# Kernel tuning notes

Measured on AMD Instinct MI355X. Metric: run time of the kernel, lower is better.

## Reference

```python
import jax, jax.numpy as jnp
import numpy as np

B = 4096
D = 2048
K = 8          # num_intention
H2 = 64        # fc2 out


def setup_inputs() -> dict:
    key = jax.random.key(0)
    ks = jax.random.split(key, 8)
    x = jax.random.normal(ks[0], (B, D), dtype=jnp.float32)
    # one-hot intention per sample
    idx = jax.random.randint(ks[1], (B,), 0, K)
    intention = jax.nn.one_hot(idx, K, dtype=jnp.float32)
    s1 = 1.0 / np.sqrt(D)
    s2 = 1.0 / np.sqrt(K)
    s3 = 1.0 / np.sqrt(D + H2)
    W1 = jax.random.uniform(ks[2], (D * K, D), jnp.float32, -s1, s1)
    b1 = jax.random.uniform(ks[3], (D * K,), jnp.float32, -s1, s1)
    W2 = jax.random.uniform(ks[4], (H2, K), jnp.float32, -s2, s2)
    b2 = jax.random.uniform(ks[5], (H2,), jnp.float32, -s2, s2)
    W3 = jax.random.uniform(ks[6], (1, D + H2), jnp.float32, -s3, s3)
    b3 = jax.random.uniform(ks[7], (1,), jnp.float32, -s3, s3)
    return {"x": x, "intention": intention, "W1": W1, "b1": b1,
            "W2": W2, "b2": b2, "W3": W3, "b3": b3}


def reference(x, intention, W1, b1, W2, b2, W3, b3):
    # fc2 on the one-hot intention -> [B, 64]
    y2 = intention @ W2.T + b2
    # fc1 densely computes all K branches (dropout treated as identity / eval mode)
    y1 = x @ W1.T + b1                      # [B, D*K]
    # mask = intention.repeat(1, 2048): branch axis is INNERMOST (interleaved)
    y1 = y1.reshape(B, D, K)                # [B, D, K]
    sel = jax.lax.stop_gradient(intention)  # mask is non-differentiable in torch
    y1 = jnp.einsum('bdk,bk->bd', y1, sel)  # gather active branch -> [B, D]
    y3 = jax.nn.relu(jnp.concatenate([y1, y2], axis=1))  # [B, D+64]
    y = y3 @ W3.T + b3                      # [B, 1]
    return y
```

## Files before the change

### kernel.cpp

```cpp
#include <hip/hip_runtime.h>
#include <hip/hip_bf16.h>
#include <stdint.h>

#define NB 4096
#define ND 2048
#define NK 8
#define NH 64

#define BM 128
#define BN 128
#define BK 32
#define MAX_ROWS 5120
#define MAX_TILES 40

typedef __bf16 bf16;
typedef __bf16 bf16x8 __attribute__((ext_vector_type(8)));
typedef float floatx4 __attribute__((ext_vector_type(4)));

#define OFF_KIDX   0u
#define OFF_ORDER  16384u
#define OFF_META   40960u
#define OFF_XG     65536u
#define OFF_WB     21037056u

__global__ void prep_kernel(const float* __restrict__ intention,
                            const float* __restrict__ W2,
                            const float* __restrict__ b2,
                            const float* __restrict__ W3,
                            const float* __restrict__ b3,
                            int* __restrict__ kidx,
                            int* __restrict__ order,
                            int* __restrict__ meta,
                            float* __restrict__ out)
{
    __shared__ int cnt[NK];
    __shared__ int cur[NK];
    __shared__ float c2s[NK];
    const int tid = threadIdx.x;

    if (tid < NK) cnt[tid] = 0;
    for (int i = tid; i < MAX_ROWS; i += 256) order[i] = -1;
    __syncthreads();

    for (int b = tid; b < NB; b += 256) {
        const float* row = intention + b * NK;
        int k = 0;
#pragma unroll
        for (int j = 1; j < NK; j++)
            if (row[j] > 0.5f) k = j;
        kidx[b] = k;
        atomicAdd(&cnt[k], 1);
    }
    __syncthreads();

    if (tid == 0) {
        int running = 0, nt = 0;
        for (int k = 0; k < NK; k++) {
            cur[k] = running;
            int ntile = (cnt[k] + BM - 1) / BM;
            for (int t = 0; t < ntile; t++) {
                meta[1 + nt] = k;
                meta[1 + MAX_TILES + nt] = running + t * BM;
                nt++;
            }
            running += ntile * BM;
        }
        meta[0] = nt;
    }
    __syncthreads();

    for (int b = tid; b < NB; b += 256) {
        int k = kidx[b];
        int pos = atomicAdd(&cur[k], 1);
        order[pos] = b;
    }

    if (tid < NK) {
        float s = b3[0];
        for (int h = 0; h < NH; h++) {
            float v = W2[h * NK + tid] + b2[h];
            if (v > 0.f) s += v * W3[ND + h];
        }
        c2s[tid] = s;
    }
    __syncthreads();

    for (int b = tid; b < NB; b += 256)
        out[b] = c2s[kidx[b]];
}

__global__ void gather_x_kernel(const float* __restrict__ x,
                                const int* __restrict__ order,
                                bf16* __restrict__ xg)
{
    const int row = blockIdx.x;
    const int t = threadIdx.x;
    const int b = order[row];
    bf16* dst = xg + (size_t)row * ND + t * 8;
    bf16x8 v;
    if (b < 0) {
#pragma unroll
        for (int i = 0; i < 8; i++) v[i] = (bf16)0.f;
    } else {
        const float* src = x + (size_t)b * ND + t * 8;
        float4 a = *(const float4*)(src);
        float4 c = *(const float4*)(src + 4);
        v[0] = (bf16)a.x; v[1] = (bf16)a.y; v[2] = (bf16)a.z; v[3] = (bf16)a.w;
        v[4] = (bf16)c.x; v[5] = (bf16)c.y; v[6] = (bf16)c.z; v[7] = (bf16)c.w;
    }
    *(bf16x8*)dst = v;
}

__global__ void conv_w1_kernel(const float* __restrict__ W1,
                               bf16* __restrict__ Wb)
{
    const int r = blockIdx.x;
    const int t = threadIdx.x;
    const int d = r >> 3;
    const int k = r & 7;
    const float* src = W1 + (size_t)r * ND + t * 8;
    bf16* dst = Wb + ((size_t)k * ND + d) * ND + t * 8;
    float4 a = *(const float4*)(src);
    float4 c = *(const float4*)(src + 4);
    bf16x8 v;
    v[0] = (bf16)a.x; v[1] = (bf16)a.y; v[2] = (bf16)a.z; v[3] = (bf16)a.w;
    v[4] = (bf16)c.x; v[5] = (bf16)c.y; v[6] = (bf16)c.z; v[7] = (bf16)c.w;
    *(bf16x8*)dst = v;
}

__global__ void gemm_kernel(const bf16* __restrict__ xg,
                            const bf16* __restrict__ Wb,
                            const int* __restrict__ order,
                            const int* __restrict__ meta,
                            const float* __restrict__ b1,
                            const float* __restrict__ W3,
                            float* __restrict__ out)
{
    const int n_mt = meta[0];
    const int mt = blockIdx.y;
    if (mt >= n_mt) return;
    const int kbr = meta[1 + mt];
    const int row0 = meta[1 + MAX_TILES + mt];
    const int col0 = blockIdx.x * BN;

    __shared__ bf16 As[BM * BK];
    __shared__ bf16 Bs[BN * BK];

    const int tid = threadIdx.x;
    const int lane = tid & 63;
    const int wid = tid >> 6;
    const int wm = wid >> 1;
    const int wn = wid & 1;

    const bf16* Abase = xg + (size_t)row0 * ND;
    const bf16* Bbase = Wb + ((size_t)kbr * ND + col0) * ND;

    const int srow = tid >> 2;
    const int scol = (tid & 3) * 8;

    floatx4 zero = {0.f, 0.f, 0.f, 0.f};
    floatx4 acc[4][4];
#pragma unroll
    for (int i = 0; i < 4; i++)
#pragma unroll
        for (int j = 0; j < 4; j++) acc[i][j] = zero;

    const int qk = (lane >> 4) * 8;
    const int mrow = lane & 15;

    for (int kk = 0; kk < ND; kk += BK) {
#pragma unroll
        for (int r = 0; r < 2; r++) {
            const bf16* ga = Abase + (size_t)(r * 64 + srow) * ND + kk + scol;
            const bf16* gb = Bbase + (size_t)(r * 64 + srow) * ND + kk + scol;
            bf16* la = As + r * 2048 + wid * 512;
            bf16* lb = Bs + r * 2048 + wid * 512;
            __builtin_amdgcn_global_load_lds(
                (const __attribute__((address_space(1))) void*)ga,
                (__attribute__((address_space(3))) void*)la, 16, 0, 0);
            __builtin_amdgcn_global_load_lds(
                (const __attribute__((address_space(1))) void*)gb,
                (__attribute__((address_space(3))) void*)lb, 16, 0, 0);
        }
        __syncthreads();

        bf16x8 af[4], bfv[4];
#pragma unroll
        for (int i = 0; i < 4; i++) {
            af[i]  = *(const bf16x8*)(As + (wm * 64 + i * 16 + mrow) * BK + qk);
            bfv[i] = *(const bf16x8*)(Bs + (wn * 64 + i * 16 + mrow) * BK + qk);
        }
#pragma unroll
        for (int i = 0; i < 4; i++)
#pragma unroll
            for (int j = 0; j < 4; j++)
                acc[i][j] = __builtin_amdgcn_mfma_f32_16x16x32_bf16(
                    af[i], bfv[j], acc[i][j], 0, 0, 0);
        __syncthreads();
    }

    const int colq = lane & 15;
    const int quad = lane >> 4;
    float bias[4], w3v[4];
#pragma unroll
    for (int j = 0; j < 4; j++) {
        int d = col0 + wn * 64 + j * 16 + colq;
        bias[j] = b1[d * NK + kbr];
        w3v[j] = W3[d];
    }
#pragma unroll
    for (int i = 0; i < 4; i++) {
#pragma unroll
        for (int r = 0; r < 4; r++) {
            float s = 0.f;
#pragma unroll
            for (int j = 0; j < 4; j++) {
                float v = acc[i][j][r] + bias[j];
                s += (v > 0.f) ? v * w3v[j] : 0.f;
            }
#pragma unroll
            for (int m = 1; m < 16; m <<= 1) s += __shfl_xor(s, m, 64);
            if (colq == 0) {
                int grow = row0 + wm * 64 + i * 16 + quad * 4 + r;
                int b = order[grow];
                if (b >= 0) atomicAdd(out + b, s);
            }
        }
    }
}

extern "C" void kernel_launch(void* const* d_in, const int* in_sizes, int n_in,
                              void* d_out, int out_size, void* d_ws, size_t ws_size,
                              hipStream_t stream)
{
    const float* x         = (const float*)d_in[0];
    const float* intention = (const float*)d_in[1];
    const float* W1        = (const float*)d_in[2];
    const float* b1        = (const float*)d_in[3];
    const float* W2        = (const float*)d_in[4];
    const float* b2        = (const float*)d_in[5];
    const float* W3        = (const float*)d_in[6];
    const float* b3        = (const float*)d_in[7];
    float* out = (float*)d_out;

    char* ws = (char*)d_ws;
    int*  kidx  = (int*)(ws + OFF_KIDX);
    int*  order = (int*)(ws + OFF_ORDER);
    int*  meta  = (int*)(ws + OFF_META);
    bf16* xg    = (bf16*)(ws + OFF_XG);
    bf16* Wb    = (bf16*)(ws + OFF_WB);

    prep_kernel<<<dim3(1), dim3(256), 0, stream>>>(
        intention, W2, b2, W3, b3, kidx, order, meta, out);
    conv_w1_kernel<<<dim3(NK * ND), dim3(256), 0, stream>>>(W1, Wb);
    gather_x_kernel<<<dim3(MAX_ROWS), dim3(256), 0, stream>>>(x, order, xg);
    gemm_kernel<<<dim3(ND / BN, MAX_TILES), dim3(256), 0, stream>>>(
        xg, Wb, order, meta, b1, W3, out);
}
```

Before: 338.0 us.

## Fuse fp32-to-bf16 conversion and row gather into GEMM tile loads

Removes the separate W1 conversion and x gather kernels; the GEMM now loads fp32 rows of x (via the sorted order) and the interleaved W1 rows directly, converts to bf16 in registers and stores into padded shared memory. This eliminates writing and rereading bf16 copies of W1 and x in global memory. It gives up the async global-to-LDS loads and reads twice the bytes per tile from fp32 sources, with W1 rows strided by the branch interleave. Shared memory rows are padded to reduce bank conflicts.

```diff
diff --git a/kernel.cpp b/kernel.cpp
--- a/kernel.cpp
+++ b/kernel.cpp
@@ -10,6 +10,7 @@
 #define BM 128
 #define BN 128
 #define BK 32
+#define LDA 40
 #define MAX_ROWS 5120
 #define MAX_TILES 40
 
@@ -20,8 +21,6 @@
 #define OFF_KIDX   0u
 #define OFF_ORDER  16384u
 #define OFF_META   40960u
-#define OFF_XG     65536u
-#define OFF_WB     21037056u
 
 __global__ void prep_kernel(const float* __restrict__ intention,
                             const float* __restrict__ W2,
@@ -89,47 +88,15 @@
         out[b] = c2s[kidx[b]];
 }
 
-__global__ void gather_x_kernel(const float* __restrict__ x,
-                                const int* __restrict__ order,
-                                bf16* __restrict__ xg)
-{
-    const int row = blockIdx.x;
-    const int t = threadIdx.x;
-    const int b = order[row];
-    bf16* dst = xg + (size_t)row * ND + t * 8;
-    bf16x8 v;
-    if (b < 0) {
-#pragma unroll
-        for (int i = 0; i < 8; i++) v[i] = (bf16)0.f;
-    } else {
-        const float* src = x + (size_t)b * ND + t * 8;
-        float4 a = *(const float4*)(src);
-        float4 c = *(const float4*)(src + 4);
-        v[0] = (bf16)a.x; v[1] = (bf16)a.y; v[2] = (bf16)a.z; v[3] = (bf16)a.w;
-        v[4] = (bf16)c.x; v[5] = (bf16)c.y; v[6] = (bf16)c.z; v[7] = (bf16)c.w;
-    }
-    *(bf16x8*)dst = v;
-}
-
-__global__ void conv_w1_kernel(const float* __restrict__ W1,
-                               bf16* __restrict__ Wb)
-{
-    const int r = blockIdx.x;
-    const int t = threadIdx.x;
-    const int d = r >> 3;
-    const int k = r & 7;
-    const float* src = W1 + (size_t)r * ND + t * 8;
-    bf16* dst = Wb + ((size_t)k * ND + d) * ND + t * 8;
-    float4 a = *(const float4*)(src);
-    float4 c = *(const float4*)(src + 4);
+__device__ inline void cvt_store16(bf16* dst, float4 a, float4 c) {
     bf16x8 v;
     v[0] = (bf16)a.x; v[1] = (bf16)a.y; v[2] = (bf16)a.z; v[3] = (bf16)a.w;
     v[4] = (bf16)c.x; v[5] = (bf16)c.y; v[6] = (bf16)c.z; v[7] = (bf16)c.w;
     *(bf16x8*)dst = v;
 }
 
-__global__ void gemm_kernel(const bf16* __restrict__ xg,
-                            const bf16* __restrict__ Wb,
+__global__ void gemm_kernel(const float* __restrict__ x,
+                            const float* __restrict__ W1,
                             const int* __restrict__ order,
                             const int* __restrict__ meta,
                             const float* __restrict__ b1,
@@ -143,8 +110,9 @@
     const int row0 = meta[1 + MAX_TILES + mt];
     const int col0 = blockIdx.x * BN;
 
-    __shared__ bf16 As[BM * BK];
-    __shared__ bf16 Bs[BN * BK];
+    __shared__ int rowb[BM];
+    __shared__ bf16 As[BM * LDA];
+    __shared__ bf16 Bs[BN * LDA];
 
     const int tid = threadIdx.x;
     const int lane = tid & 63;
@@ -152,12 +120,23 @@
     const int wm = wid >> 1;
     const int wn = wid & 1;
 
-    const bf16* Abase = xg + (size_t)row0 * ND;
-    const bf16* Bbase = Wb + ((size_t)kbr * ND + col0) * ND;
+    if (tid < BM) rowb[tid] = order[row0 + tid];
+    __syncthreads();
 
     const int srow = tid >> 2;
     const int scol = (tid & 3) * 8;
 
+    const int a0 = rowb[srow];
+    const int a1 = rowb[64 + srow];
+    const float* pa0 = x + (size_t)(a0 < 0 ? 0 : a0) * ND + scol;
+    const float* pa1 = x + (size_t)(a1 < 0 ? 0 : a1) * ND + scol;
+    const float* pb0 = W1 + ((size_t)(col0 + srow) * NK + kbr) * ND + scol;
+    const float* pb1 = W1 + ((size_t)(col0 + 64 + srow) * NK + kbr) * ND + scol;
+    bf16* wa0 = As + srow * LDA + scol;
+    bf16* wa1 = As + (64 + srow) * LDA + scol;
+    bf16* wb0 = Bs + srow * LDA + scol;
+    bf16* wb1 = Bs + (64 + srow) * LDA + scol;
+
     floatx4 zero = {0.f, 0.f, 0.f, 0.f};
     floatx4 acc[4][4];
 #pragma unroll
@@ -169,26 +148,25 @@
     const int mrow = lane & 15;
 
     for (int kk = 0; kk < ND; kk += BK) {
-#pragma unroll
-        for (int r = 0; r < 2; r++) {
-            const bf16* ga = Abase + (size_t)(r * 64 + srow) * ND + kk + scol;
-            const bf16* gb = Bbase + (size_t)(r * 64 + srow) * ND + kk + scol;
-            bf16* la = As + r * 2048 + wid * 512;
-            bf16* lb = Bs + r * 2048 + wid * 512;
-            __builtin_amdgcn_global_load_lds(
-                (const __attribute__((address_space(1))) void*)ga,
-                (__attribute__((address_space(3))) void*)la, 16, 0, 0);
-            __builtin_amdgcn_global_load_lds(
-                (const __attribute__((address_space(1))) void*)gb,
-                (__attribute__((address_space(3))) void*)lb, 16, 0, 0);
-        }
+        float4 va0 = *(const float4*)(pa0 + kk);
+        float4 va0b = *(const float4*)(pa0 + kk + 4);
+        float4 va1 = *(const float4*)(pa1 + kk);
+        float4 va1b = *(const float4*)(pa1 + kk + 4);
+        float4 vb0 = *(const float4*)(pb0 + kk);
+        float4 vb0b = *(const float4*)(pb0 + kk + 4);
+        float4 vb1 = *(const float4*)(pb1 + kk);
+        float4 vb1b = *(const float4*)(pb1 + kk + 4);
+        cvt_store16(wa0, va0, va0b);
+        cvt_store16(wa1, va1, va1b);
+        cvt_store16(wb0, vb0, vb0b);
+        cvt_store16(wb1, vb1, vb1b);
         __syncthreads();
 
         bf16x8 af[4], bfv[4];
 #pragma unroll
         for (int i = 0; i < 4; i++) {
-            af[i]  = *(const bf16x8*)(As + (wm * 64 + i * 16 + mrow) * BK + qk);
-            bfv[i] = *(const bf16x8*)(Bs + (wn * 64 + i * 16 + mrow) * BK + qk);
+            af[i]  = *(const bf16x8*)(As + (wm * 64 + i * 16 + mrow) * LDA + qk);
+            bfv[i] = *(const bf16x8*)(Bs + (wn * 64 + i * 16 + mrow) * LDA + qk);
         }
 #pragma unroll
         for (int i = 0; i < 4; i++)
@@ -221,8 +199,7 @@
 #pragma unroll
             for (int m = 1; m < 16; m <<= 1) s += __shfl_xor(s, m, 64);
             if (colq == 0) {
-                int grow = row0 + wm * 64 + i * 16 + quad * 4 + r;
-                int b = order[grow];
+                int b = rowb[wm * 64 + i * 16 + quad * 4 + r];
                 if (b >= 0) atomicAdd(out + b, s);
             }
         }
@@ -247,13 +224,9 @@
     int*  kidx  = (int*)(ws + OFF_KIDX);
     int*  order = (int*)(ws + OFF_ORDER);
     int*  meta  = (int*)(ws + OFF_META);
-    bf16* xg    = (bf16*)(ws + OFF_XG);
-    bf16* Wb    = (bf16*)(ws + OFF_WB);
 
     prep_kernel<<<dim3(1), dim3(256), 0, stream>>>(
         intention, W2, b2, W3, b3, kidx, order, meta, out);
-    conv_w1_kernel<<<dim3(NK * ND), dim3(256), 0, stream>>>(W1, Wb);
-    gather_x_kernel<<<dim3(MAX_ROWS), dim3(256), 0, stream>>>(x, order, xg);
     gemm_kernel<<<dim3(ND / BN, MAX_TILES), dim3(256), 0, stream>>>(
-        xg, Wb, order, meta, b1, W3, out);
-}
+        x, W1, order, meta, b1, W3, out);
+}
```

New measurement: 360.7 us. 1.07x slower.

## Split prep into parallel kernels and use fragment-ordered LDS tile layout

Applied to the files above, without the earlier changes.

Replaces the single-block prep kernel with three kernels: a parallel one-hot decode, a small metadata and constant kernel, and a parallel scatter that fills the row order and initial outputs. The GEMM now stores A and B tiles in LDS in MFMA-fragment order, so each lane reads a contiguous 16-byte chunk, which is meant to avoid bank conflicts from the strided row layout. Row-to-sample indices are cached in shared memory for the epilogue, and several bounds clamps are added. The cost is two extra kernel launches plus some defensive checks.

```diff
diff --git a/kernel.cpp b/kernel.cpp
--- a/kernel.cpp
+++ b/kernel.cpp
@@ -20,45 +20,71 @@
 #define OFF_KIDX   0u
 #define OFF_ORDER  16384u
 #define OFF_META   40960u
+#define OFF_CUR    41472u
+#define OFF_C2S    41536u
 #define OFF_XG     65536u
 #define OFF_WB     21037056u
 
-__global__ void prep_kernel(const float* __restrict__ intention,
+__global__ void kidx_kernel(const float* __restrict__ intention,
+                            int* __restrict__ kidx,
+                            int* __restrict__ order)
+{
+    const int b = blockIdx.x * 256 + threadIdx.x;
+    float4 a = *(const float4*)(intention + (size_t)b * NK);
+    float4 c = *(const float4*)(intention + (size_t)b * NK + 4);
+    int k = 0;
+    if (a.y > 0.5f) k = 1;
+    if (a.z > 0.5f) k = 2;
+    if (a.w > 0.5f) k = 3;
+    if (c.x > 0.5f) k = 4;
+    if (c.y > 0.5f) k = 5;
+    if (c.z > 0.5f) k = 6;
+    if (c.w > 0.5f) k = 7;
+    kidx[b] = k;
+    order[b] = -1;
+    if (b < MAX_ROWS - NB) order[NB + b] = -1;
+}
+
+__global__ void meta_kernel(const int* __restrict__ kidx,
                             const float* __restrict__ W2,
                             const float* __restrict__ b2,
                             const float* __restrict__ W3,
                             const float* __restrict__ b3,
-                            int* __restrict__ kidx,
-                            int* __restrict__ order,
                             int* __restrict__ meta,
-                            float* __restrict__ out)
+                            int* __restrict__ cursors,
+                            float* __restrict__ c2s)
 {
     __shared__ int cnt[NK];
-    __shared__ int cur[NK];
-    __shared__ float c2s[NK];
     const int tid = threadIdx.x;
-
     if (tid < NK) cnt[tid] = 0;
-    for (int i = tid; i < MAX_ROWS; i += 256) order[i] = -1;
     __syncthreads();
 
-    for (int b = tid; b < NB; b += 256) {
-        const float* row = intention + b * NK;
-        int k = 0;
-#pragma unroll
-        for (int j = 1; j < NK; j++)
-            if (row[j] > 0.5f) k = j;
-        kidx[b] = k;
-        atomicAdd(&cnt[k], 1);
+    for (int i = tid; i < NB; i += 256)
+        atomicAdd(&cnt[kidx[i] & 7], 1);
+
+    if (tid < 64) {
+        const int k = tid & 7;
+        const int hc = tid >> 3;
+        float s = 0.f;
+#pragma unroll
+        for (int j = 0; j < 8; j++) {
+            int h = hc * 8 + j;
+            float v = W2[h * NK + k] + b2[h];
+            if (v > 0.f) s += v * W3[ND + h];
+        }
+        s += __shfl_xor(s, 8, 64);
+        s += __shfl_xor(s, 16, 64);
+        s += __shfl_xor(s, 32, 64);
+        if (tid < 8) c2s[k] = s + b3[0];
     }
     __syncthreads();
 
     if (tid == 0) {
         int running = 0, nt = 0;
         for (int k = 0; k < NK; k++) {
-            cur[k] = running;
+            cursors[k] = running;
             int ntile = (cnt[k] + BM - 1) / BM;
-            for (int t = 0; t < ntile; t++) {
+            for (int t = 0; t < ntile && nt < MAX_TILES; t++) {
                 meta[1 + nt] = k;
                 meta[1 + MAX_TILES + nt] = running + t * BM;
                 nt++;
@@ -67,26 +93,19 @@
         }
         meta[0] = nt;
     }
-    __syncthreads();
-
-    for (int b = tid; b < NB; b += 256) {
-        int k = kidx[b];
-        int pos = atomicAdd(&cur[k], 1);
-        order[pos] = b;
-    }
-
-    if (tid < NK) {
-        float s = b3[0];
-        for (int h = 0; h < NH; h++) {
-            float v = W2[h * NK + tid] + b2[h];
-            if (v > 0.f) s += v * W3[ND + h];
-        }
-        c2s[tid] = s;
-    }
-    __syncthreads();
-
-    for (int b = tid; b < NB; b += 256)
-        out[b] = c2s[kidx[b]];
+}
+
+__global__ void scatter_kernel(const int* __restrict__ kidx,
+                               int* __restrict__ cursors,
+                               const float* __restrict__ c2s,
+                               int* __restrict__ order,
+                               float* __restrict__ out)
+{
+    const int b = blockIdx.x * 256 + threadIdx.x;
+    const int k = kidx[b] & 7;
+    const int pos = atomicAdd(&cursors[k], 1);
+    if (pos >= 0 && pos < MAX_ROWS) order[pos] = b;
+    out[b] = c2s[k];
 }
 
 __global__ void gather_x_kernel(const float* __restrict__ x,
@@ -98,7 +117,7 @@
     const int b = order[row];
     bf16* dst = xg + (size_t)row * ND + t * 8;
     bf16x8 v;
-    if (b < 0) {
+    if (b < 0 || b >= NB) {
 #pragma unroll
         for (int i = 0; i < 8; i++) v[i] = (bf16)0.f;
     } else {
@@ -128,23 +147,28 @@
     *(bf16x8*)dst = v;
 }
 
-__global__ void gemm_kernel(const bf16* __restrict__ xg,
-                            const bf16* __restrict__ Wb,
-                            const int* __restrict__ order,
-                            const int* __restrict__ meta,
-                            const float* __restrict__ b1,
-                            const float* __restrict__ W3,
-                            float* __restrict__ out)
-{
-    const int n_mt = meta[0];
+__global__ void __launch_bounds__(256)
+gemm_kernel(const bf16* __restrict__ xg,
+            const bf16* __restrict__ Wb,
+            const int* __restrict__ order,
+            const int* __restrict__ meta,
+            const float* __restrict__ b1,
+            const float* __restrict__ W3,
+            float* __restrict__ out)
+{
+    int n_mt = meta[0];
+    if (n_mt > MAX_TILES) n_mt = MAX_TILES;
     const int mt = blockIdx.y;
     if (mt >= n_mt) return;
-    const int kbr = meta[1 + mt];
-    const int row0 = meta[1 + MAX_TILES + mt];
+    const int kbr = meta[1 + mt] & 7;
+    int row0 = meta[1 + MAX_TILES + mt];
+    if (row0 < 0) row0 = 0;
+    if (row0 > MAX_ROWS - BM) row0 = MAX_ROWS - BM;
     const int col0 = blockIdx.x * BN;
 
     __shared__ bf16 As[BM * BK];
     __shared__ bf16 Bs[BN * BK];
+    __shared__ int rowb[BM];
 
     const int tid = threadIdx.x;
     const int lane = tid & 63;
@@ -152,11 +176,18 @@
     const int wm = wid >> 1;
     const int wn = wid & 1;
 
-    const bf16* Abase = xg + (size_t)row0 * ND;
-    const bf16* Bbase = Wb + ((size_t)kbr * ND + col0) * ND;
-
-    const int srow = tid >> 2;
-    const int scol = (tid & 3) * 8;
+    if (tid < BM) rowb[tid] = order[row0 + tid];
+
+    const int fr = lane & 15;
+    const int fq = lane >> 4;
+    const bf16* gA0 = xg + (size_t)(row0 + wid * 32 + fr) * ND + fq * 8;
+    const bf16* gA1 = gA0 + (size_t)16 * ND;
+    const bf16* gB0 = Wb + ((size_t)kbr * ND + col0 + wid * 32 + fr) * ND + fq * 8;
+    const bf16* gB1 = gB0 + (size_t)16 * ND;
+    bf16* lA0 = As + (wid * 2) * 512;
+    bf16* lA1 = As + (wid * 2 + 1) * 512;
+    bf16* lB0 = Bs + (wid * 2) * 512;
+    bf16* lB1 = Bs + (wid * 2 + 1) * 512;
 
     floatx4 zero = {0.f, 0.f, 0.f, 0.f};
     floatx4 acc[4][4];
@@ -165,30 +196,26 @@
 #pragma unroll
         for (int j = 0; j < 4; j++) acc[i][j] = zero;
 
-    const int qk = (lane >> 4) * 8;
-    const int mrow = lane & 15;
-
     for (int kk = 0; kk < ND; kk += BK) {
-#pragma unroll
-        for (int r = 0; r < 2; r++) {
-            const bf16* ga = Abase + (size_t)(r * 64 + srow) * ND + kk + scol;
-            const bf16* gb = Bbase + (size_t)(r * 64 + srow) * ND + kk + scol;
-            bf16* la = As + r * 2048 + wid * 512;
-            bf16* lb = Bs + r * 2048 + wid * 512;
-            __builtin_amdgcn_global_load_lds(
-                (const __attribute__((address_space(1))) void*)ga,
-                (__attribute__((address_space(3))) void*)la, 16, 0, 0);
-            __builtin_amdgcn_global_load_lds(
-                (const __attribute__((address_space(1))) void*)gb,
-                (__attribute__((address_space(3))) void*)lb, 16, 0, 0);
-        }
+        __builtin_amdgcn_global_load_lds(
+            (const __attribute__((address_space(1))) void*)(gA0 + kk),
+            (__attribute__((address_space(3))) void*)lA0, 16, 0, 0);
+        __builtin_amdgcn_global_load_lds(
+            (const __attribute__((address_space(1))) void*)(gA1 + kk),
+            (__attribute__((address_space(3))) void*)lA1, 16, 0, 0);
+        __builtin_amdgcn_global_load_lds(
+            (const __attribute__((address_space(1))) void*)(gB0 + kk),
+            (__attribute__((address_space(3))) void*)lB0, 16, 0, 0);
+        __builtin_amdgcn_global_load_lds(
+            (const __attribute__((address_space(1))) void*)(gB1 + kk),
+            (__attribute__((address_space(3))) void*)lB1, 16, 0, 0);
         __syncthreads();
 
         bf16x8 af[4], bfv[4];
 #pragma unroll
         for (int i = 0; i < 4; i++) {
-            af[i]  = *(const bf16x8*)(As + (wm * 64 + i * 16 + mrow) * BK + qk);
-            bfv[i] = *(const bf16x8*)(Bs + (wn * 64 + i * 16 + mrow) * BK + qk);
+            af[i]  = *(const bf16x8*)(As + (wm * 4 + i) * 512 + lane * 8);
+            bfv[i] = *(const bf16x8*)(Bs + (wn * 4 + i) * 512 + lane * 8);
         }
 #pragma unroll
         for (int i = 0; i < 4; i++)
@@ -221,9 +248,8 @@
 #pragma unroll
             for (int m = 1; m < 16; m <<= 1) s += __shfl_xor(s, m, 64);
             if (colq == 0) {
-                int grow = row0 + wm * 64 + i * 16 + quad * 4 + r;
-                int b = order[grow];
-                if (b >= 0) atomicAdd(out + b, s);
+                int b = rowb[wm * 64 + i * 16 + quad * 4 + r];
+                if (b >= 0 && b < NB) atomicAdd(out + b, s);
             }
         }
     }
@@ -244,14 +270,19 @@
     float* out = (float*)d_out;
 
     char* ws = (char*)d_ws;
-    int*  kidx  = (int*)(ws + OFF_KIDX);
-    int*  order = (int*)(ws + OFF_ORDER);
-    int*  meta  = (int*)(ws + OFF_META);
-    bf16* xg    = (bf16*)(ws + OFF_XG);
-    bf16* Wb    = (bf16*)(ws + OFF_WB);
-
-    prep_kernel<<<dim3(1), dim3(256), 0, stream>>>(
-        intention, W2, b2, W3, b3, kidx, order, meta, out);
+    int*   kidx    = (int*)(ws + OFF_KIDX);
+    int*   order   = (int*)(ws + OFF_ORDER);
+    int*   meta    = (int*)(ws + OFF_META);
+    int*   cursors = (int*)(ws + OFF_CUR);
+    float* c2s     = (float*)(ws + OFF_C2S);
+    bf16*  xg      = (bf16*)(ws + OFF_XG);
+    bf16*  Wb      = (bf16*)(ws + OFF_WB);
+
+    kidx_kernel<<<dim3(16), dim3(256), 0, stream>>>(intention, kidx, order);
+    meta_kernel<<<dim3(1), dim3(256), 0, stream>>>(
+        kidx, W2, b2, W3, b3, meta, cursors, c2s);
+    scatter_kernel<<<dim3(16), dim3(256), 0, stream>>>(
+        kidx, cursors, c2s, order, out);
     conv_w1_kernel<<<dim3(NK * ND), dim3(256), 0, stream>>>(W1, Wb);
     gather_x_kernel<<<dim3(MAX_ROWS), dim3(256), 0, stream>>>(x, order, xg);
     gemm_kernel<<<dim3(ND / BN, MAX_TILES), dim3(256), 0, stream>>>(
```

Result: slower. 363.0 us (+7.4%).
